# Performance work log

Hardware: AMD Instinct MI355X
Metric: run time of the kernel (lower is better)

## Reference

```python
import jax, jax.numpy as jnp
import numpy as np

B, T, H, V = 64, 256, 1024, 1000


def setup_inputs() -> dict:
    key = jax.random.key(0)
    ks = jax.random.split(key, 6)
    s = 1.0 / np.sqrt(V + H)
    return {
        "enc_h": jax.random.normal(ks[0], (B, H), jnp.float32),
        "enc_c": jax.random.normal(ks[1], (B, H), jnp.float32),
        "trg_in": jax.random.randint(ks[2], (B, T), 0, V),
        "W_w": jax.random.normal(ks[3], (4 * H, V + H), jnp.float32) * s,
        "W_b": jnp.zeros((4 * H,), jnp.float32),
        "fc_w": jax.random.normal(ks[4], (V, H), jnp.float32) * (1.0 / np.sqrt(H)),
        "fc_b": jnp.zeros((V,), jnp.float32),
    }


def reference(enc_h, enc_c, trg_in, W_w, W_b, fc_w, fc_b):
    # Deterministic eval mode: teacher_forcing_ratio=1.0, dropout off.
    # Input at step t is one_hot(trg_in[:, t]).
    x = jax.nn.one_hot(trg_in, V, dtype=jnp.float32)  # [B, T, V]
    xs = jnp.transpose(x, (1, 0, 2))  # [T, B, V]

    def step(carry, x_t):
        h, c = carry
        z = jnp.concatenate([x_t, h], axis=1)  # [B, V+H]
        gates = z @ W_w.T + W_b  # [B, 4H]
        i, f, g, o = jnp.split(gates, 4, axis=1)
        i = jax.nn.sigmoid(i)
        f = jax.nn.sigmoid(f)
        g = jnp.tanh(g)
        o = jax.nn.sigmoid(o)
        c_t = f * c + i * g
        h_t = o * jnp.tanh(c_t)
        logits = h_t @ fc_w.T + fc_b  # [B, V]
        return (h_t, c_t), logits

    (_, _), logits = jax.lax.scan(step, (enc_h, enc_c), xs)
    return jnp.transpose(logits, (1, 0, 2))  # [B, T, V]
```

## Files before the change

### kernel.cpp

```cpp
#include <hip/hip_runtime.h>


#define TT 256
#define NH 1024
#define NV 1000
#define WROW 2024
#define NGRP 4
#define GPW 64
#define GB 16

typedef __attribute__((ext_vector_type(8))) short short8;
typedef __attribute__((ext_vector_type(8))) _Float16 half8;
typedef __attribute__((ext_vector_type(4))) float f32x4;

#define AGT __HIP_MEMORY_SCOPE_AGENT

__device__ __forceinline__ unsigned short f2bf(float f) {
    unsigned int u = __float_as_uint(f);
    u += 0x7fffu + ((u >> 16) & 1u);
    return (unsigned short)(u >> 16);
}
__device__ __forceinline__ float bf2f(unsigned short s) {
    return __uint_as_float(((unsigned int)s) << 16);
}
__device__ __forceinline__ unsigned short f2h(float f) {
    return __builtin_bit_cast(unsigned short, (_Float16)f);
}
__device__ __forceinline__ half8 as_h8(short8 s) {
    return __builtin_bit_cast(half8, s);
}
__device__ __forceinline__ float sigm(float x) {
    return __builtin_amdgcn_rcpf(1.0f + __expf(-x));
}
__device__ __forceinline__ float tanh_f(float x) {
    return 2.0f * __builtin_amdgcn_rcpf(1.0f + __expf(-2.0f * x)) - 1.0f;
}

__global__ void embT_kernel(const float* __restrict__ Ww, unsigned short* __restrict__ embT) {
    __shared__ unsigned short tile[64][80];
    const int rt = blockIdx.x & 63, vt = blockIdx.x >> 6;
    const int r0 = rt * 64, v0 = vt * 64;
    const int t = threadIdx.x;
    {
        int rr = t >> 2, c0 = (t & 3) * 16;
        for (int j = 0; j < 16; ++j) {
            int v = v0 + c0 + j;
            float x = (v < NV) ? Ww[(size_t)(r0 + rr) * WROW + v] : 0.f;
            tile[c0 + j][rr] = f2bf(x);
        }
    }
    __syncthreads();
    {
        int vv = t >> 2, k0 = (t & 3) * 16;
        int v = v0 + vv;
        if (v < NV)
            for (int j = 0; j < 16; ++j)
                embT[(size_t)v * 4096 + r0 + k0 + j] = tile[vv][k0 + j];
    }
}

__global__ void h0_kernel(const float* __restrict__ enc_h, unsigned short* __restrict__ hring,
                          int ring) {
    int i = blockIdx.x * 256 + threadIdx.x;
    int b = i >> 10, u = i & 1023;
    int g = b >> 4, bl = b & 15;
    hring[(size_t)g * ring * 16384 + ((u >> 4) << 8) + (bl << 4) + (u & 15)] = f2h(enc_h[i]);
}

template <int RING, int FCAD>
__global__ void __launch_bounds__(256, 1)
lstm_kernel(const float* __restrict__ enc_c,
            const int* __restrict__ trg,
            const float* __restrict__ Ww,
            const float* __restrict__ Wb,
            const float* __restrict__ fcw,
            const float* __restrict__ fcb,
            const unsigned short* __restrict__ embT,
            unsigned short* __restrict__ hring,
            int* __restrict__ syn,
            float* __restrict__ out) {
    __shared__ unsigned short smw[65536];
    __shared__ float gl[4][4][16][18];
    __shared__ unsigned short ht[16][20];

    const int pb = blockIdx.x;
    const int xcd = pb & 7;
    const int g = xcd >> 1;
    const int iw = ((xcd & 1) << 5) + (pb >> 3);
    const int tid = threadIdx.x;
    const int wv = tid >> 6;
    const int lane = tid & 63;
    const int ml = lane & 15;
    const int kq = lane >> 4;
    const int kl8 = kq * 8;
    const int rq = kq * 4;
    const int gB = g * GB;
    int* gfl4 = syn + g * 64;
    unsigned short* hbase = hring + (size_t)g * RING * 16384;

    const int u0 = iw * 16;
    for (int c = tid; c < 8192; c += 256) {
        int row = c >> 7;
        int col8 = (c & 127) << 3;
        int grow = ((row >> 4) << 10) + u0 + (row & 15);
        const float* src = Ww + (size_t)grow * WROW + 1000 + col8;
        float4 a = *(const float4*)src;
        float4 b2 = *(const float4*)(src + 4);
        union { unsigned short us[8]; short8 s; } w;
        w.us[0] = f2h(a.x); w.us[1] = f2h(a.y); w.us[2] = f2h(a.z); w.us[3] = f2h(a.w);
        w.us[4] = f2h(b2.x); w.us[5] = f2h(b2.y); w.us[6] = f2h(b2.z); w.us[7] = f2h(b2.w);
        int byt = ((c & 127) << 4) ^ ((row & 7) << 4);
        *(short8*)(smw + (row << 10) + (byt >> 1)) = w.s;
    }
    const int v0 = iw * 16;
    const int vrowc = (v0 + ml < NV) ? v0 + ml : NV - 1;
    half8 la[8];
    #pragma unroll
    for (int j = 0; j < 8; ++j) {
        const float* src = fcw + (size_t)vrowc * NH + (((wv << 3) + j) << 5) + kl8;
        union { unsigned short us[8]; short8 s; } w;
        #pragma unroll
        for (int e = 0; e < 8; ++e) w.us[e] = f2h(src[e]);
        la[j] = as_h8(w.s);
    }
    const int b = tid & 15;
    const int u = tid >> 4;
    float bs[4];
    #pragma unroll
    for (int q = 0; q < 4; ++q)
        bs[q] = Wb[(q << 10) + u0 + u];
    float creg = enc_c[(size_t)(gB + b) * NH + u0 + u];
    const int srow = (tid & 63) >> 2, sseg = tid & 3;
    float fbs[4];
    #pragma unroll
    for (int r = 0; r < 4; ++r) {
        int v = v0 + (sseg << 2) + r;
        fbs[r] = fcb[v < NV ? v : NV - 1];
    }
    __syncthreads();

    for (int p = 1; p <= TT + 1; ++p) {
        unsigned short emb[4];
        if (p <= TT) {
            int idx = trg[(gB + b) * TT + p - 1];
            #pragma unroll
            for (int q = 0; q < 4; ++q)
                emb[q] = embT[(size_t)idx * 4096 + (q << 10) + u0 + u];
        }
        if (tid < 64) {
            if (FCAD == 1 || (p & (FCAD - 1)) == 1)
                __builtin_amdgcn_fence(__ATOMIC_ACQUIRE, "agent");
            if (p > 1)
                while (__hip_atomic_load(gfl4 + tid, __ATOMIC_RELAXED, AGT) < p - 1) { }
        }
        __syncthreads();

        const unsigned short* hh = hbase + (size_t)((p - 1) & (RING - 1)) * 16384;
        half8 hb[8];
        #pragma unroll
        for (int j = 0; j < 8; ++j) {
            int wgp = (wv << 4) + (j << 1) + (kq >> 1);
            hb[j] = as_h8(*(const short8*)(hh + (wgp << 8) + (ml << 4) + ((kq & 1) << 3)));
        }

        if (p <= TT) {
            f32x4 acc[4] = {};
            #pragma unroll
            for (int j = 0; j < 8; ++j) {
                int kb = (((wv << 3) + j) << 5) + kl8;
                #pragma unroll
                for (int rt = 0; rt < 4; ++rt) {
                    int row = (rt << 4) + ml;
                    int byt = (kb << 1) ^ ((row & 7) << 4);
                    half8 a = as_h8(*(const short8*)(smw + (row << 10) + (byt >> 1)));
                    acc[rt] = __builtin_amdgcn_mfma_f32_16x16x32_f16(a, hb[j], acc[rt], 0, 0, 0);
                }
            }
            #pragma unroll
            for (int rt = 0; rt < 4; ++rt)
                #pragma unroll
                for (int r = 0; r < 4; ++r)
                    gl[wv][rt][rq + r][ml] = acc[rt][r];
            __syncthreads();
            float pre[4];
            #pragma unroll
            for (int q = 0; q < 4; ++q)
                pre[q] = gl[0][q][u][b] + gl[1][q][u][b] + gl[2][q][u][b] + gl[3][q][u][b]
                         + bs[q] + bf2f(emb[q]);
            float ii = sigm(pre[0]), ff = sigm(pre[1]);
            float gg = tanh_f(pre[2]), oo = sigm(pre[3]);
            float cc = ff * creg + ii * gg;
            creg = cc;
            ht[b][u] = f2h(oo * tanh_f(cc));
            __syncthreads();
            if (tid < 32) {
                int b2 = tid >> 1, u8 = (tid & 1) << 3;
                unsigned long long lo = *(const unsigned long long*)&ht[b2][u8];
                unsigned long long hi;
                memcpy(&hi, &ht[b2][u8 + 4], 8);
                unsigned short* dst = hbase + (size_t)(p & (RING - 1)) * 16384
                                      + (iw << 8) + (b2 << 4) + u8;
                __hip_atomic_store((unsigned long long*)dst, lo, __ATOMIC_RELAXED, AGT);
                __hip_atomic_store((unsigned long long*)(dst + 4), hi, __ATOMIC_RELAXED, AGT);
                asm volatile("s_waitcnt vmcnt(0)" ::: "memory");
                if (tid == 0)
                    __hip_atomic_store(gfl4 + iw, p, __ATOMIC_RELAXED, AGT);
            }
        }

        if (p >= 2) {
            f32x4 accl = {};
            #pragma unroll
            for (int j = 0; j < 8; ++j)
                accl = __builtin_amdgcn_mfma_f32_16x16x32_f16(la[j], hb[j], accl, 0, 0, 0);
            #pragma unroll
            for (int r = 0; r < 4; ++r)
                gl[wv][0][rq + r][ml] = accl[r];
            __syncthreads();
            if (tid >= 64 && tid < 128) {
                int vq = v0 + (sseg << 2);
                f32x4 val;
                #pragma unroll
                for (int r = 0; r < 4; ++r) {
                    int rowi = (sseg << 2) + r;
                    val[r] = gl[0][0][rowi][srow] + gl[1][0][rowi][srow]
                           + gl[2][0][rowi][srow] + gl[3][0][rowi][srow] + fbs[r];
                }
                float* po = out + ((size_t)(gB + srow) * TT + (p - 2)) * NV + vq;
                if (vq + 3 < NV) {
                    __builtin_nontemporal_store(val, (f32x4*)po);
                } else {
                    #pragma unroll
                    for (int r = 0; r < 4; ++r)
                        if (vq + r < NV) __builtin_nontemporal_store(val[r], po + r);
                }
            }
        }
    }
}

extern "C" void kernel_launch(void* const* d_in, const int* in_sizes, int n_in,
                              void* d_out, int out_size, void* d_ws, size_t ws_size,
                              hipStream_t stream) {
    const float* enc_h = (const float*)d_in[0];
    const float* enc_c = (const float*)d_in[1];
    const int* trg = (const int*)d_in[2];
    const float* Ww = (const float*)d_in[3];
    const float* Wb = (const float*)d_in[4];
    const float* fcw = (const float*)d_in[5];
    const float* fcb = (const float*)d_in[6];
    float* out = (float*)d_out;

    unsigned short* embT = (unsigned short*)d_ws;
    unsigned short* hring = embT + (size_t)1000 * 4096;

    const size_t embBytes = (size_t)1000 * 4096 * 2;
    const size_t slotBytes = (size_t)16384 * 2;
    const size_t need16 = embBytes + (size_t)NGRP * 16 * slotBytes + 8192;

    hipLaunchKernelGGL(embT_kernel, dim3(1024), dim3(256), 0, stream, Ww, embT);

    if (ws_size >= need16) {
        int* syn = (int*)(hring + (size_t)NGRP * 16 * 16384);
        hipMemsetAsync(syn, 0, 4096, stream);
        hipLaunchKernelGGL(h0_kernel, dim3(256), dim3(256), 0, stream, enc_h, hring, 16);
        lstm_kernel<16, 8><<<dim3(NGRP * GPW), dim3(256), 0, stream>>>(
            enc_c, trg, Ww, Wb, fcw, fcb, embT, hring, syn, out);
    } else {
        int* syn = (int*)(hring + (size_t)NGRP * 4 * 16384);
        hipMemsetAsync(syn, 0, 4096, stream);
        hipLaunchKernelGGL(h0_kernel, dim3(256), dim3(256), 0, stream, enc_h, hring, 4);
        lstm_kernel<4, 1><<<dim3(NGRP * GPW), dim3(256), 0, stream>>>(
            enc_c, trg, Ww, Wb, fcw, fcb, embT, hring, syn, out);
    }
}
```

Baseline: 840.1 us.

## Spin-wait in every wave and do LSTM cell update in one wave

```diff
diff --git a/kernel.cpp b/kernel.cpp
--- a/kernel.cpp
+++ b/kernel.cpp
@@ -81,7 +81,7 @@
             float* __restrict__ out) {
     __shared__ unsigned short smw[65536];
     __shared__ float gl[4][4][16][18];
-    __shared__ unsigned short ht[16][20];
+    __shared__ float glo[4][16][18];
 
     const int pb = blockIdx.x;
     const int xcd = pb & 7;
@@ -123,14 +123,19 @@
         for (int e = 0; e < 8; ++e) w.us[e] = f2h(src[e]);
         la[j] = as_h8(w.s);
     }
-    const int b = tid & 15;
-    const int u = tid >> 4;
-    float bs[4];
+    const int pb_ = lane >> 2;
+    const int pu = (lane & 3) << 2;
+    float bs4[4][4];
     #pragma unroll
     for (int q = 0; q < 4; ++q)
-        bs[q] = Wb[(q << 10) + u0 + u];
-    float creg = enc_c[(size_t)(gB + b) * NH + u0 + u];
-    const int srow = (tid & 63) >> 2, sseg = tid & 3;
+        #pragma unroll
+        for (int j = 0; j < 4; ++j)
+            bs4[q][j] = Wb[(q << 10) + u0 + pu + j];
+    float creg4[4];
+    #pragma unroll
+    for (int j = 0; j < 4; ++j)
+        creg4[j] = enc_c[(size_t)(gB + pb_) * NH + u0 + pu + j];
+    const int srow = lane >> 2, sseg = lane & 3;
     float fbs[4];
     #pragma unroll
     for (int r = 0; r < 4; ++r) {
@@ -140,20 +145,22 @@
     __syncthreads();
 
     for (int p = 1; p <= TT + 1; ++p) {
-        unsigned short emb[4];
-        if (p <= TT) {
-            int idx = trg[(gB + b) * TT + p - 1];
+        unsigned short emb4[4][4];
+        if (wv == 0 && p <= TT) {
+            int idx = trg[(gB + pb_) * TT + p - 1];
             #pragma unroll
             for (int q = 0; q < 4; ++q)
-                emb[q] = embT[(size_t)idx * 4096 + (q << 10) + u0 + u];
-        }
-        if (tid < 64) {
-            if (FCAD == 1 || (p & (FCAD - 1)) == 1)
-                __builtin_amdgcn_fence(__ATOMIC_ACQUIRE, "agent");
-            if (p > 1)
-                while (__hip_atomic_load(gfl4 + tid, __ATOMIC_RELAXED, AGT) < p - 1) { }
-        }
-        __syncthreads();
+                #pragma unroll
+                for (int j = 0; j < 4; ++j)
+                    emb4[q][j] = embT[(size_t)idx * 4096 + (q << 10) + u0 + pu + j];
+        }
+        if (FCAD == 1 || (p & (FCAD - 1)) == 1)
+            __builtin_amdgcn_fence(__ATOMIC_ACQUIRE, "agent");
+        if (p > 1) {
+            const int* f = gfl4 + (wv << 4) + (lane & 15);
+            while (__hip_atomic_load(f, __ATOMIC_RELAXED, AGT) < p - 1) { }
+        }
+        asm volatile("" ::: "memory");
 
         const unsigned short* hh = hbase + (size_t)((p - 1) & (RING - 1)) * 16384;
         half8 hb[8];
@@ -162,9 +169,8 @@
             int wgp = (wv << 4) + (j << 1) + (kq >> 1);
             hb[j] = as_h8(*(const short8*)(hh + (wgp << 8) + (ml << 4) + ((kq & 1) << 3)));
         }
-
+        f32x4 acc[4] = {};
         if (p <= TT) {
-            f32x4 acc[4] = {};
             #pragma unroll
             for (int j = 0; j < 8; ++j) {
                 int kb = (((wv << 3) + j) << 5) + kl8;
@@ -176,36 +182,39 @@
                     acc[rt] = __builtin_amdgcn_mfma_f32_16x16x32_f16(a, hb[j], acc[rt], 0, 0, 0);
                 }
             }
+        }
+        __syncthreads();
+        if (p <= TT) {
             #pragma unroll
             for (int rt = 0; rt < 4; ++rt)
                 #pragma unroll
                 for (int r = 0; r < 4; ++r)
                     gl[wv][rt][rq + r][ml] = acc[rt][r];
-            __syncthreads();
-            float pre[4];
-            #pragma unroll
-            for (int q = 0; q < 4; ++q)
-                pre[q] = gl[0][q][u][b] + gl[1][q][u][b] + gl[2][q][u][b] + gl[3][q][u][b]
-                         + bs[q] + bf2f(emb[q]);
-            float ii = sigm(pre[0]), ff = sigm(pre[1]);
-            float gg = tanh_f(pre[2]), oo = sigm(pre[3]);
-            float cc = ff * creg + ii * gg;
-            creg = cc;
-            ht[b][u] = f2h(oo * tanh_f(cc));
-            __syncthreads();
-            if (tid < 32) {
-                int b2 = tid >> 1, u8 = (tid & 1) << 3;
-                unsigned long long lo = *(const unsigned long long*)&ht[b2][u8];
-                unsigned long long hi;
-                memcpy(&hi, &ht[b2][u8 + 4], 8);
-                unsigned short* dst = hbase + (size_t)(p & (RING - 1)) * 16384
-                                      + (iw << 8) + (b2 << 4) + u8;
-                __hip_atomic_store((unsigned long long*)dst, lo, __ATOMIC_RELAXED, AGT);
-                __hip_atomic_store((unsigned long long*)(dst + 4), hi, __ATOMIC_RELAXED, AGT);
-                asm volatile("s_waitcnt vmcnt(0)" ::: "memory");
-                if (tid == 0)
-                    __hip_atomic_store(gfl4 + iw, p, __ATOMIC_RELAXED, AGT);
+        }
+        __syncthreads();
+
+        if (p <= TT && wv == 0) {
+            unsigned long long hw = 0;
+            #pragma unroll
+            for (int j = 0; j < 4; ++j) {
+                int u = pu + j;
+                float pre[4];
+                #pragma unroll
+                for (int q = 0; q < 4; ++q)
+                    pre[q] = gl[0][q][u][pb_] + gl[1][q][u][pb_] + gl[2][q][u][pb_]
+                           + gl[3][q][u][pb_] + bs4[q][j] + bf2f(emb4[q][j]);
+                float ii = sigm(pre[0]), ff = sigm(pre[1]);
+                float gg = tanh_f(pre[2]), oo = sigm(pre[3]);
+                float cc = ff * creg4[j] + ii * gg;
+                creg4[j] = cc;
+                hw |= (unsigned long long)f2h(oo * tanh_f(cc)) << (j * 16);
             }
+            unsigned short* dst = hbase + (size_t)(p & (RING - 1)) * 16384
+                                  + (iw << 8) + (lane << 2);
+            __hip_atomic_store((unsigned long long*)dst, hw, __ATOMIC_RELAXED, AGT);
+            asm volatile("s_waitcnt vmcnt(0)" ::: "memory");
+            if (lane == 0)
+                __hip_atomic_store(gfl4 + iw, p, __ATOMIC_RELAXED, AGT);
         }
 
         if (p >= 2) {
@@ -215,16 +224,16 @@
                 accl = __builtin_amdgcn_mfma_f32_16x16x32_f16(la[j], hb[j], accl, 0, 0, 0);
             #pragma unroll
             for (int r = 0; r < 4; ++r)
-                gl[wv][0][rq + r][ml] = accl[r];
+                glo[wv][rq + r][ml] = accl[r];
             __syncthreads();
-            if (tid >= 64 && tid < 128) {
+            if (wv == 1) {
                 int vq = v0 + (sseg << 2);
                 f32x4 val;
                 #pragma unroll
                 for (int r = 0; r < 4; ++r) {
                     int rowi = (sseg << 2) + r;
-                    val[r] = gl[0][0][rowi][srow] + gl[1][0][rowi][srow]
-                           + gl[2][0][rowi][srow] + gl[3][0][rowi][srow] + fbs[r];
+                    val[r] = glo[0][rowi][srow] + glo[1][rowi][srow]
+                           + glo[2][rowi][srow] + glo[3][rowi][srow] + fbs[r];
                 }
                 float* po = out + ((size_t)(gB + srow) * TT + (p - 2)) * NV + vq;
                 if (vq + 3 < NV) {
```

Result: slower. 1.144 ms (+36.1%).
